# Performance work log

Measured on AMD Instinct MI355X. Metric: run time of the kernel, lower is better.

The kernel has to match this reference:

```python
import jax, jax.numpy as jnp
import numpy as np

T, B, D = 1024, 8, 1024
H, DH = 16, 64  # n_head, d_inner; H*DH == D
EPS = 1e-5


def setup_inputs() -> dict:
    key = jax.random.key(0)
    ks = jax.random.split(key, 8)
    q = jax.random.normal(ks[0], (T, B, D), dtype=jnp.float32)
    k = jax.random.normal(ks[1], (T, B, D), dtype=jnp.float32)
    v = jax.random.normal(ks[2], (T, B, D), dtype=jnp.float32)
    # causal mask: True where attention is disallowed (j > i)
    attn_mask = jnp.triu(jnp.ones((T, T), dtype=bool), k=1)
    Wq = jax.random.normal(ks[3], (D, H * DH), dtype=jnp.float32) * 0.02
    Wk = jax.random.normal(ks[4], (D, H * DH), dtype=jnp.float32) * 0.02
    Wv = jax.random.normal(ks[5], (D, H * DH), dtype=jnp.float32) * 0.02
    Wo = jax.random.normal(ks[6], (H * DH, D), dtype=jnp.float32) * 0.02
    gamma = jnp.ones((D,), dtype=jnp.float32)
    beta = jnp.zeros((D,), dtype=jnp.float32)
    return {"q": q, "k": k, "v": v, "attn_mask": attn_mask,
            "Wq": Wq, "Wk": Wk, "Wv": Wv, "Wo": Wo,
            "gamma": gamma, "beta": beta}


def _layer_norm(x, gamma, beta):
    mu = jnp.mean(x, axis=-1, keepdims=True)
    var = jnp.mean(jnp.square(x - mu), axis=-1, keepdims=True)
    return (x - mu) * jax.lax.rsqrt(var + EPS) * gamma + beta


def reference(q, k, v, attn_mask, Wq, Wk, Wv, Wo, gamma, beta):
    Tq, bsz, _ = q.shape
    Tk = k.shape[0]
    scale = 1.0 / (DH ** 0.5)
    # post-LN path (pre_lnorm=False): project raw inputs
    hq = (q @ Wq).reshape(Tq, bsz, H, DH)
    hk = (k @ Wk).reshape(Tk, bsz, H, DH)
    hv = (v @ Wv).reshape(Tk, bsz, H, DH)
    # explicit [Tq, Tk, B, H] score tensor, as in original
    score = jnp.einsum('ibhd,jbhd->ijbh', hq, hk) * scale
    score = jnp.where(attn_mask[:, :, None, None], -jnp.inf, score)
    prob = jax.nn.softmax(score, axis=1)  # softmax over key dim j
    vec = jnp.einsum('ijbh,jbhd->ibhd', prob, hv).reshape(Tq, bsz, H * DH)
    attn_out = vec @ Wo
    return _layer_norm(attn_out, gamma, beta)
```

## Files before the change

### kernel.cpp

```cpp
#include <hip/hip_runtime.h>
#include <hip/hip_bf16.h>


typedef __bf16 bf16x8 __attribute__((ext_vector_type(8)));
typedef float f32x4 __attribute__((ext_vector_type(4)));
typedef float f32x16 __attribute__((ext_vector_type(16)));
typedef unsigned short ushort8_t __attribute__((ext_vector_type(8)));

__device__ __forceinline__ unsigned short f2bf(float f) {
  unsigned int u = __builtin_bit_cast(unsigned int, f);
  u += 0x7FFFu + ((u >> 16) & 1u);
  return (unsigned short)(u >> 16);
}

__device__ __forceinline__ unsigned int cvt_pk_bf16(float lo, float hi) {
  unsigned int r;
  asm("v_cvt_pk_bf16_f32 %0, %1, %2" : "=v"(r) : "v"(lo), "v"(hi));
  return r;
}

__device__ __forceinline__ void gl2lds16(const unsigned short* g, unsigned short* l) {
  __builtin_amdgcn_global_load_lds(
      (const __attribute__((address_space(1))) void*)g,
      (__attribute__((address_space(3))) void*)l, 16, 0, 0);
}

template<int EPI>
__global__ __launch_bounds__(256)
void gemm_bf16(const unsigned short* __restrict__ A,
               const unsigned short* __restrict__ Bt,
               void* __restrict__ C)
{
  __shared__ __align__(16) unsigned short As[2][128 * 64];
  __shared__ __align__(16) unsigned short Bs[2][128 * 64];
  const int tid = threadIdx.x;
  const int lane = tid & 63, wid = tid >> 6;
  const int wr = wid >> 1, wc = wid & 1;
  const int l15 = lane & 15, l4 = lane >> 4;
  const int bm = blockIdx.x, bn = blockIdx.y;

  f32x4 acc[4][4];
#pragma unroll
  for (int m = 0; m < 4; ++m)
#pragma unroll
    for (int n = 0; n < 4; ++n)
      acc[m][n] = (f32x4){0.f, 0.f, 0.f, 0.f};

  const unsigned short* ga = A  + (size_t)bm * 128 * 1024 + (tid >> 3) * 1024 + (tid & 7) * 8;
  const unsigned short* gb = Bt + (size_t)bn * 128 * 1024 + (tid >> 3) * 1024 + (tid & 7) * 8;
  const int ldsoff = wid * 512;

#pragma unroll
  for (int i = 0; i < 4; ++i) {
    gl2lds16(ga + i * 32 * 1024, &As[0][ldsoff + i * 2048]);
    gl2lds16(gb + i * 32 * 1024, &Bs[0][ldsoff + i * 2048]);
  }

  int cur = 0;
  for (int kt = 0; kt < 1024; kt += 64) {
    __syncthreads();
    if (kt + 64 < 1024) {
#pragma unroll
      for (int i = 0; i < 4; ++i) {
        gl2lds16(ga + i * 32 * 1024 + kt + 64, &As[cur ^ 1][ldsoff + i * 2048]);
        gl2lds16(gb + i * 32 * 1024 + kt + 64, &Bs[cur ^ 1][ldsoff + i * 2048]);
      }
    }
#pragma unroll
    for (int kk = 0; kk < 2; ++kk) {
      bf16x8 af[4], bfr[4];
#pragma unroll
      for (int m = 0; m < 4; ++m)
        af[m] = *(const bf16x8*)(&As[cur][(wr * 64 + m * 16 + l15) * 64 + kk * 32 + l4 * 8]);
#pragma unroll
      for (int n = 0; n < 4; ++n)
        bfr[n] = *(const bf16x8*)(&Bs[cur][(wc * 64 + n * 16 + l15) * 64 + kk * 32 + l4 * 8]);
#pragma unroll
      for (int m = 0; m < 4; ++m)
#pragma unroll
        for (int n = 0; n < 4; ++n)
          acc[m][n] = __builtin_amdgcn_mfma_f32_16x16x32_bf16(af[m], bfr[n], acc[m][n], 0, 0, 0);
    }
    cur ^= 1;
  }

#pragma unroll
  for (int m = 0; m < 4; ++m)
#pragma unroll
    for (int n = 0; n < 4; ++n)
#pragma unroll
      for (int r = 0; r < 4; ++r) {
        int row = bm * 128 + wr * 64 + m * 16 + l4 * 4 + r;
        int col = bn * 128 + wc * 64 + n * 16 + l15;
        float v = acc[m][n][r];
        if constexpr (EPI == 2) {
          ((float*)C)[(size_t)row * 1024 + col] = v;
        } else {
          int t = row >> 3, b = row & 7;
          int h = col >> 6, dh = col & 63;
          size_t base = ((size_t)(b * 16 + h)) << 16;
          ((unsigned short*)C)[base + (size_t)dh * 1024 + t] = f2bf(v);
        }
      }
}

__global__ __launch_bounds__(256)
void gemm_qk(const unsigned short* __restrict__ Aq, const unsigned short* __restrict__ Ak,
             const unsigned short* __restrict__ Wq, const unsigned short* __restrict__ Wk,
             unsigned short* __restrict__ Cq, unsigned short* __restrict__ Ck)
{
  const int z = blockIdx.z;
  const unsigned short* A  = z ? Ak : Aq;
  const unsigned short* Bt = z ? Wk : Wq;
  unsigned short* C        = z ? Ck : Cq;
  __shared__ __align__(16) unsigned short As[128 * 64];
  __shared__ __align__(16) unsigned short Bs[128 * 64];
  const int tid = threadIdx.x;
  const int lane = tid & 63, wid = tid >> 6;
  const int wr = wid >> 1, wc = wid & 1;
  const int l15 = lane & 15, l4 = lane >> 4;
  const int bm = blockIdx.x, bn = blockIdx.y;

  f32x4 acc[4][4];
#pragma unroll
  for (int m = 0; m < 4; ++m)
#pragma unroll
    for (int n = 0; n < 4; ++n)
      acc[m][n] = (f32x4){0.f, 0.f, 0.f, 0.f};

  const unsigned short* ga = A  + (size_t)bm * 128 * 1024 + (tid >> 3) * 1024 + (tid & 7) * 8;
  const unsigned short* gb = Bt + (size_t)bn * 128 * 1024 + (tid >> 3) * 1024 + (tid & 7) * 8;
  unsigned short* la = As + wid * 512;
  unsigned short* lb = Bs + wid * 512;

  for (int kt = 0; kt < 1024; kt += 64) {
    if (kt) __syncthreads();
#pragma unroll
    for (int i = 0; i < 4; ++i) {
      gl2lds16(ga + i * 32 * 1024 + kt, la + i * 2048);
      gl2lds16(gb + i * 32 * 1024 + kt, lb + i * 2048);
    }
    __syncthreads();
#pragma unroll
    for (int kk = 0; kk < 2; ++kk) {
      bf16x8 af[4], bfr[4];
#pragma unroll
      for (int m = 0; m < 4; ++m)
        af[m] = *(const bf16x8*)(As + (wr * 64 + m * 16 + l15) * 64 + kk * 32 + l4 * 8);
#pragma unroll
      for (int n = 0; n < 4; ++n)
        bfr[n] = *(const bf16x8*)(Bs + (wc * 64 + n * 16 + l15) * 64 + kk * 32 + l4 * 8);
#pragma unroll
      for (int m = 0; m < 4; ++m)
#pragma unroll
        for (int n = 0; n < 4; ++n)
          acc[m][n] = __builtin_amdgcn_mfma_f32_16x16x32_bf16(af[m], bfr[n], acc[m][n], 0, 0, 0);
    }
  }

#pragma unroll
  for (int m = 0; m < 4; ++m)
#pragma unroll
    for (int n = 0; n < 4; ++n)
#pragma unroll
      for (int r = 0; r < 4; ++r) {
        int row = bm * 128 + wr * 64 + m * 16 + l4 * 4 + r;
        int col = bn * 128 + wc * 64 + n * 16 + l15;
        int t = row >> 3, b = row & 7;
        int h = col >> 6, dh = col & 63;
        size_t base = ((size_t)(b * 16 + h)) << 16;
        C[base + (size_t)t * 64 + dh] = f2bf(acc[m][n][r]);
      }
}

__global__ __launch_bounds__(256)
void conv_bf16(const float* __restrict__ in, unsigned short* __restrict__ out)
{
  size_t i = ((size_t)blockIdx.x * 256 + threadIdx.x) * 8;
  float4 a = *(const float4*)(in + i);
  float4 b = *(const float4*)(in + i + 4);
  ushort8_t o;
  o[0] = f2bf(a.x); o[1] = f2bf(a.y); o[2] = f2bf(a.z); o[3] = f2bf(a.w);
  o[4] = f2bf(b.x); o[5] = f2bf(b.y); o[6] = f2bf(b.z); o[7] = f2bf(b.w);
  *(ushort8_t*)(out + i) = o;
}

__global__ __launch_bounds__(256)
void conv2_bf16(const float* __restrict__ in0, const float* __restrict__ in1,
                unsigned short* __restrict__ out0, unsigned short* __restrict__ out1)
{
  const float* in = blockIdx.y ? in1 : in0;
  unsigned short* out = blockIdx.y ? out1 : out0;
  size_t i = ((size_t)blockIdx.x * 256 + threadIdx.x) * 8;
  float4 a = *(const float4*)(in + i);
  float4 b = *(const float4*)(in + i + 4);
  ushort8_t o;
  o[0] = f2bf(a.x); o[1] = f2bf(a.y); o[2] = f2bf(a.z); o[3] = f2bf(a.w);
  o[4] = f2bf(b.x); o[5] = f2bf(b.y); o[6] = f2bf(b.z); o[7] = f2bf(b.w);
  *(ushort8_t*)(out + i) = o;
}

__global__ __launch_bounds__(256)
void wconv4(const float* __restrict__ W0, const float* __restrict__ W1,
            const float* __restrict__ W2, const float* __restrict__ W3,
            unsigned short* __restrict__ T0, unsigned short* __restrict__ T1,
            unsigned short* __restrict__ T2, unsigned short* __restrict__ T3)
{
  const int y = blockIdx.y;
  const float* W = y == 0 ? W0 : y == 1 ? W1 : y == 2 ? W2 : W3;
  unsigned short* Wt = y == 0 ? T0 : y == 1 ? T1 : y == 2 ? T2 : T3;
  const float scale = (y == 0) ? 0.125f * 1.44269504088896f : 1.0f;
  int id = blockIdx.x * 256 + threadIdx.x;
  int n = id & 1023;
  int k0 = (id >> 10) << 3;
  ushort8_t o;
#pragma unroll
  for (int j = 0; j < 8; ++j)
    o[j] = f2bf(W[(size_t)(k0 + j) * 1024 + n] * scale);
  *(ushort8_t*)(Wt + (size_t)n * 1024 + k0) = o;
}

__global__ __launch_bounds__(256)
void flash_attn(const unsigned short* __restrict__ hq,
                const unsigned short* __restrict__ hk,
                const unsigned short* __restrict__ hvt,
                unsigned short* __restrict__ vec)
{
  __shared__ __align__(16) unsigned short Ks[2][64 * 64];
  __shared__ __align__(16) unsigned short Vs[2][64 * 64];
  const int tid = threadIdx.x;
  const int lane = tid & 63, wid = tid >> 6;
  const int l31 = lane & 31, h = lane >> 5;
  const int h8 = h * 8, h4 = h * 4;
  const int swz = l31 & 7;
  const int bid = blockIdx.x;
  const int xcd = bid & 7;
  const int i = bid >> 3;
  const int bh = (xcd << 4) | (i & 15);
  const int qb = 7 - (i >> 4);
  const int tau = qb * 4 + wid;
  const int b = bh >> 4, hh = bh & 15;
  const size_t base = (size_t)bh << 16;
  const int qrow = tau * 32 + l31;

  const int srow = wid * 8 + (lane >> 3);
  const int sc16 = (lane & 7) ^ (srow & 7);
  const unsigned short* gk = hk  + base + (size_t)srow * 64 + sc16 * 8;
  const unsigned short* gv = hvt + base + (size_t)srow * 1024 + sc16 * 8;
  const int ldst = wid * 512;

  bf16x8 qf[4];
#pragma unroll
  for (int ks = 0; ks < 4; ++ks)
    qf[ks] = *(const bf16x8*)(hq + base + (size_t)qrow * 64 + ks * 16 + h8);

  f32x16 of0, of1;
#pragma unroll
  for (int r = 0; r < 16; ++r) { of0[r] = 0.f; of1[r] = 0.f; }
  float mrun = -3.0e38f, lrun = 0.f;

  const int nblk = 2 * qb + 2;
  const int myend = (4 * qb + wid) >> 1;

  gl2lds16(gk,                 &Ks[0][ldst]);
  gl2lds16(gk + 32 * 64,       &Ks[0][2048 + ldst]);
  gl2lds16(gv,                 &Vs[0][ldst]);
  gl2lds16(gv + 32 * 1024,     &Vs[0][2048 + ldst]);

  int cur = 0;
  for (int kt = 0; kt < nblk; ++kt) {
    __syncthreads();
    if (kt + 1 < nblk) {
      const int kvb1 = (kt + 1) * 64;
      gl2lds16(gk + (size_t)kvb1 * 64,             &Ks[cur ^ 1][ldst]);
      gl2lds16(gk + (size_t)(kvb1 + 32) * 64,      &Ks[cur ^ 1][2048 + ldst]);
      gl2lds16(gv + kvb1,                          &Vs[cur ^ 1][ldst]);
      gl2lds16(gv + 32 * 1024 + kvb1,              &Vs[cur ^ 1][2048 + ldst]);
    }
    if (kt <= myend) {
      const int kvb = kt * 64;
      f32x16 sa, sb;
#pragma unroll
      for (int r = 0; r < 16; ++r) { sa[r] = 0.f; sb[r] = 0.f; }
      __builtin_amdgcn_s_setprio(1);
#pragma unroll
      for (int ks = 0; ks < 4; ++ks) {
        const int c = ((ks * 2 + h) ^ swz) << 3;
        bf16x8 kfa = *(const bf16x8*)(&Ks[cur][l31 * 64 + c]);
        bf16x8 kfb = *(const bf16x8*)(&Ks[cur][(32 + l31) * 64 + c]);
        sa = __builtin_amdgcn_mfma_f32_32x32x16_bf16(kfa, qf[ks], sa, 0, 0, 0);
        sb = __builtin_amdgcn_mfma_f32_32x32x16_bf16(kfb, qf[ks], sb, 0, 0, 0);
      }
      __builtin_amdgcn_s_setprio(0);
      if (kt == myend) {
#pragma unroll
        for (int r = 0; r < 16; ++r) {
          int kv = kvb + (r & 3) + 8 * (r >> 2) + h4;
          if (kv > qrow) sa[r] = -1.0e30f;
          if (kv + 32 > qrow) sb[r] = -1.0e30f;
        }
      }
      float mx[8];
#pragma unroll
      for (int g = 0; g < 4; ++g) {
        mx[g]     = fmaxf(fmaxf(sa[4 * g], sa[4 * g + 1]), fmaxf(sa[4 * g + 2], sa[4 * g + 3]));
        mx[4 + g] = fmaxf(fmaxf(sb[4 * g], sb[4 * g + 1]), fmaxf(sb[4 * g + 2], sb[4 * g + 3]));
      }
      mx[0] = fmaxf(mx[0], mx[1]); mx[2] = fmaxf(mx[2], mx[3]);
      mx[4] = fmaxf(mx[4], mx[5]); mx[6] = fmaxf(mx[6], mx[7]);
      float mloc = fmaxf(fmaxf(mx[0], mx[2]), fmaxf(mx[4], mx[6]));
      mloc = fmaxf(mloc, __shfl_xor(mloc, 32));
      if (!__all(mloc <= mrun + 8.0f)) {
        float mnew = fmaxf(mrun, mloc);
        float alpha = __builtin_amdgcn_exp2f(mrun - mnew);
        mrun = mnew;
        lrun *= alpha;
#pragma unroll
        for (int r = 0; r < 16; ++r) { of0[r] *= alpha; of1[r] *= alpha; }
      }
      bf16x8 pa[4];
      float lsum = 0.f;
#pragma unroll
      for (int s2 = 0; s2 < 4; ++s2) {
        float p0 = __builtin_amdgcn_exp2f(((s2 < 2) ? sa[8 * s2 + 0] : sb[8 * (s2 - 2) + 0]) - mrun);
        float p1 = __builtin_amdgcn_exp2f(((s2 < 2) ? sa[8 * s2 + 1] : sb[8 * (s2 - 2) + 1]) - mrun);
        float p2 = __builtin_amdgcn_exp2f(((s2 < 2) ? sa[8 * s2 + 2] : sb[8 * (s2 - 2) + 2]) - mrun);
        float p3 = __builtin_amdgcn_exp2f(((s2 < 2) ? sa[8 * s2 + 3] : sb[8 * (s2 - 2) + 3]) - mrun);
        float p4 = __builtin_amdgcn_exp2f(((s2 < 2) ? sa[8 * s2 + 4] : sb[8 * (s2 - 2) + 4]) - mrun);
        float p5 = __builtin_amdgcn_exp2f(((s2 < 2) ? sa[8 * s2 + 5] : sb[8 * (s2 - 2) + 5]) - mrun);
        float p6 = __builtin_amdgcn_exp2f(((s2 < 2) ? sa[8 * s2 + 6] : sb[8 * (s2 - 2) + 6]) - mrun);
        float p7 = __builtin_amdgcn_exp2f(((s2 < 2) ? sa[8 * s2 + 7] : sb[8 * (s2 - 2) + 7]) - mrun);
        lsum += (p0 + p1) + (p2 + p3) + ((p4 + p5) + (p6 + p7));
        uint4 w4 = make_uint4(cvt_pk_bf16(p0, p1), cvt_pk_bf16(p2, p3),
                              cvt_pk_bf16(p4, p5), cvt_pk_bf16(p6, p7));
        pa[s2] = __builtin_bit_cast(bf16x8, w4);
      }
      lsum += __shfl_xor(lsum, 32);
      lrun += lsum;
      __builtin_amdgcn_s_setprio(1);
#pragma unroll
      for (int s2 = 0; s2 < 4; ++s2) {
        const int c1 = (((2 * s2)     ^ swz) << 3) + h4;
        const int c2 = (((2 * s2 + 1) ^ swz) << 3) + h4;
        uint2 a1 = *(const uint2*)(&Vs[cur][l31 * 64 + c1]);
        uint2 a2 = *(const uint2*)(&Vs[cur][l31 * 64 + c2]);
        uint2 b1 = *(const uint2*)(&Vs[cur][(32 + l31) * 64 + c1]);
        uint2 b2 = *(const uint2*)(&Vs[cur][(32 + l31) * 64 + c2]);
        bf16x8 vf0 = __builtin_bit_cast(bf16x8, make_uint4(a1.x, a1.y, a2.x, a2.y));
        bf16x8 vf1 = __builtin_bit_cast(bf16x8, make_uint4(b1.x, b1.y, b2.x, b2.y));
        of0 = __builtin_amdgcn_mfma_f32_32x32x16_bf16(vf0, pa[s2], of0, 0, 0, 0);
        of1 = __builtin_amdgcn_mfma_f32_32x32x16_bf16(vf1, pa[s2], of1, 0, 0, 0);
      }
      __builtin_amdgcn_s_setprio(0);
    }
    cur ^= 1;
  }

  float rl = __builtin_amdgcn_rcpf(lrun);
  unsigned short* vout = vec + ((size_t)qrow * 8 + b) * 1024 + hh * 64;
#pragma unroll
  for (int g = 0; g < 4; ++g) {
    ushort4 o;
    o.x = f2bf(of0[g * 4 + 0] * rl); o.y = f2bf(of0[g * 4 + 1] * rl);
    o.z = f2bf(of0[g * 4 + 2] * rl); o.w = f2bf(of0[g * 4 + 3] * rl);
    *(ushort4*)(vout + 8 * g + h4) = o;
    o.x = f2bf(of1[g * 4 + 0] * rl); o.y = f2bf(of1[g * 4 + 1] * rl);
    o.z = f2bf(of1[g * 4 + 2] * rl); o.w = f2bf(of1[g * 4 + 3] * rl);
    *(ushort4*)(vout + 32 + 8 * g + h4) = o;
  }
}

__global__ __launch_bounds__(256)
void ln_inplace(float* __restrict__ x, const float* __restrict__ gamma,
                const float* __restrict__ beta)
{
  __shared__ float red[2][4];
  const int tid = threadIdx.x;
  const int lane = tid & 63, wid = tid >> 6;
  const size_t row = blockIdx.x;
  float4 v = *(const float4*)(x + row * 1024 + tid * 4);
  float s = v.x + v.y + v.z + v.w;
  float q = v.x * v.x + v.y * v.y + v.z * v.z + v.w * v.w;
#pragma unroll
  for (int m = 1; m <= 32; m <<= 1) {
    s += __shfl_xor(s, m);
    q += __shfl_xor(q, m);
  }
  if (lane == 0) { red[0][wid] = s; red[1][wid] = q; }
  __syncthreads();
  float ts = red[0][0] + red[0][1] + red[0][2] + red[0][3];
  float tq = red[1][0] + red[1][1] + red[1][2] + red[1][3];
  float mu = ts * (1.0f / 1024.0f);
  float var = tq * (1.0f / 1024.0f) - mu * mu;
  float rs = rsqrtf(var + 1e-5f);
  float4 g  = *(const float4*)(gamma + tid * 4);
  float4 bt = *(const float4*)(beta + tid * 4);
  v.x = (v.x - mu) * rs * g.x + bt.x;
  v.y = (v.y - mu) * rs * g.y + bt.y;
  v.z = (v.z - mu) * rs * g.z + bt.z;
  v.w = (v.w - mu) * rs * g.w + bt.w;
  *(float4*)(x + row * 1024 + tid * 4) = v;
}

extern "C" void kernel_launch(void* const* d_in, const int* in_sizes, int n_in,
                              void* d_out, int out_size, void* d_ws, size_t ws_size,
                              hipStream_t stream) {
  const float* q     = (const float*)d_in[0];
  const float* k     = (const float*)d_in[1];
  const float* v     = (const float*)d_in[2];
  const float* Wq    = (const float*)d_in[4];
  const float* Wk    = (const float*)d_in[5];
  const float* Wv    = (const float*)d_in[6];
  const float* Wo    = (const float*)d_in[7];
  const float* gamma = (const float*)d_in[8];
  const float* beta  = (const float*)d_in[9];

  unsigned short* ws = (unsigned short*)d_ws;
  const size_t MSZ = (size_t)8192 * 1024;
  unsigned short* hq   = ws;
  unsigned short* hk   = ws + MSZ;
  unsigned short* hvt  = ws + 2 * MSZ;
  unsigned short* tmp  = ws + 3 * MSZ;
  unsigned short* qb16 = ws + 4 * MSZ;
  unsigned short* WqT  = ws + 5 * MSZ;
  unsigned short* WkT  = WqT + 1048576;
  unsigned short* WvT  = WqT + 2097152;
  unsigned short* WoT  = WqT + 3145728;
  float* out = (float*)d_out;

  dim3 bb(256);
  dim3 gg(64, 8);
  wconv4<<<dim3(512, 4), bb, 0, stream>>>(Wq, Wk, Wv, Wo, WqT, WkT, WvT, WoT);

  conv_bf16<<<4096, bb, 0, stream>>>(v, tmp);
  gemm_bf16<1><<<gg, bb, 0, stream>>>(tmp, WvT, hvt);

  conv2_bf16<<<dim3(4096, 2), bb, 0, stream>>>(q, k, qb16, tmp);
  gemm_qk<<<dim3(64, 8, 2), bb, 0, stream>>>(qb16, tmp, WqT, WkT, hq, hk);

  flash_attn<<<1024, bb, 0, stream>>>(hq, hk, hvt, qb16);

  gemm_bf16<2><<<gg, bb, 0, stream>>>(qb16, WoT, out);
  ln_inplace<<<8192, bb, 0, stream>>>(out, gamma, beta);
}
```

Measured before the change: 210.6 us.

## Swizzle GEMM LDS layout and use 64-row tiles for V and output GEMMs

```diff
diff --git a/kernel.cpp b/kernel.cpp
--- a/kernel.cpp
+++ b/kernel.cpp
@@ -25,18 +25,22 @@
       (__attribute__((address_space(3))) void*)l, 16, 0, 0);
 }
 
-template<int EPI>
-__global__ __launch_bounds__(256)
-void gemm_bf16(const unsigned short* __restrict__ A,
-               const unsigned short* __restrict__ Bt,
-               void* __restrict__ C)
-{
-  __shared__ __align__(16) unsigned short As[2][128 * 64];
-  __shared__ __align__(16) unsigned short Bs[2][128 * 64];
+__global__ __launch_bounds__(256)
+void gemm_qk(const unsigned short* __restrict__ Aq, const unsigned short* __restrict__ Ak,
+             const unsigned short* __restrict__ Wq, const unsigned short* __restrict__ Wk,
+             unsigned short* __restrict__ Cq, unsigned short* __restrict__ Ck)
+{
+  const int z = blockIdx.z;
+  const unsigned short* A  = z ? Ak : Aq;
+  const unsigned short* Bt = z ? Wk : Wq;
+  unsigned short* C        = z ? Ck : Cq;
+  __shared__ __align__(16) unsigned short As[128 * 64];
+  __shared__ __align__(16) unsigned short Bs[128 * 64];
   const int tid = threadIdx.x;
   const int lane = tid & 63, wid = tid >> 6;
   const int wr = wid >> 1, wc = wid & 1;
   const int l15 = lane & 15, l4 = lane >> 4;
+  const int r7 = l15 & 7;
   const int bm = blockIdx.x, bn = blockIdx.y;
 
   f32x4 acc[4][4];
@@ -46,42 +50,36 @@
     for (int n = 0; n < 4; ++n)
       acc[m][n] = (f32x4){0.f, 0.f, 0.f, 0.f};
 
-  const unsigned short* ga = A  + (size_t)bm * 128 * 1024 + (tid >> 3) * 1024 + (tid & 7) * 8;
-  const unsigned short* gb = Bt + (size_t)bn * 128 * 1024 + (tid >> 3) * 1024 + (tid & 7) * 8;
-  const int ldsoff = wid * 512;
-
-#pragma unroll
-  for (int i = 0; i < 4; ++i) {
-    gl2lds16(ga + i * 32 * 1024, &As[0][ldsoff + i * 2048]);
-    gl2lds16(gb + i * 32 * 1024, &Bs[0][ldsoff + i * 2048]);
-  }
-
-  int cur = 0;
+  const int sc16 = (tid & 7) ^ ((tid >> 3) & 7);
+  const unsigned short* ga = A  + (size_t)bm * 128 * 1024 + (tid >> 3) * 1024 + sc16 * 8;
+  const unsigned short* gb = Bt + (size_t)bn * 128 * 1024 + (tid >> 3) * 1024 + sc16 * 8;
+  unsigned short* la = As + wid * 512;
+  unsigned short* lb = Bs + wid * 512;
+
   for (int kt = 0; kt < 1024; kt += 64) {
+    if (kt) __syncthreads();
+#pragma unroll
+    for (int i = 0; i < 4; ++i) {
+      gl2lds16(ga + i * 32 * 1024 + kt, la + i * 2048);
+      gl2lds16(gb + i * 32 * 1024 + kt, lb + i * 2048);
+    }
     __syncthreads();
-    if (kt + 64 < 1024) {
-#pragma unroll
-      for (int i = 0; i < 4; ++i) {
-        gl2lds16(ga + i * 32 * 1024 + kt + 64, &As[cur ^ 1][ldsoff + i * 2048]);
-        gl2lds16(gb + i * 32 * 1024 + kt + 64, &Bs[cur ^ 1][ldsoff + i * 2048]);
-      }
-    }
 #pragma unroll
     for (int kk = 0; kk < 2; ++kk) {
       bf16x8 af[4], bfr[4];
+      const int c = ((kk * 4 + l4) ^ r7) << 3;
 #pragma unroll
       for (int m = 0; m < 4; ++m)
-        af[m] = *(const bf16x8*)(&As[cur][(wr * 64 + m * 16 + l15) * 64 + kk * 32 + l4 * 8]);
+        af[m] = *(const bf16x8*)(As + (wr * 64 + m * 16 + l15) * 64 + c);
 #pragma unroll
       for (int n = 0; n < 4; ++n)
-        bfr[n] = *(const bf16x8*)(&Bs[cur][(wc * 64 + n * 16 + l15) * 64 + kk * 32 + l4 * 8]);
+        bfr[n] = *(const bf16x8*)(Bs + (wc * 64 + n * 16 + l15) * 64 + c);
 #pragma unroll
       for (int m = 0; m < 4; ++m)
 #pragma unroll
         for (int n = 0; n < 4; ++n)
           acc[m][n] = __builtin_amdgcn_mfma_f32_16x16x32_bf16(af[m], bfr[n], acc[m][n], 0, 0, 0);
     }
-    cur ^= 1;
   }
 
 #pragma unroll
@@ -91,6 +89,76 @@
 #pragma unroll
       for (int r = 0; r < 4; ++r) {
         int row = bm * 128 + wr * 64 + m * 16 + l4 * 4 + r;
+        int col = bn * 128 + wc * 64 + n * 16 + l15;
+        int t = row >> 3, b = row & 7;
+        int h = col >> 6, dh = col & 63;
+        size_t base = ((size_t)(b * 16 + h)) << 16;
+        C[base + (size_t)t * 64 + dh] = f2bf(acc[m][n][r]);
+      }
+}
+
+template<int EPI>
+__global__ __launch_bounds__(256)
+void gemm_small(const unsigned short* __restrict__ A,
+                const unsigned short* __restrict__ Bt,
+                void* __restrict__ C)
+{
+  __shared__ __align__(16) unsigned short As[64 * 64];
+  __shared__ __align__(16) unsigned short Bs[128 * 64];
+  const int tid = threadIdx.x;
+  const int lane = tid & 63, wid = tid >> 6;
+  const int wr = wid >> 1, wc = wid & 1;
+  const int l15 = lane & 15, l4 = lane >> 4;
+  const int r7 = l15 & 7;
+  const int bm = blockIdx.x, bn = blockIdx.y;
+
+  f32x4 acc[2][4];
+#pragma unroll
+  for (int m = 0; m < 2; ++m)
+#pragma unroll
+    for (int n = 0; n < 4; ++n)
+      acc[m][n] = (f32x4){0.f, 0.f, 0.f, 0.f};
+
+  const int sc16 = (tid & 7) ^ ((tid >> 3) & 7);
+  const unsigned short* ga = A  + (size_t)bm * 64 * 1024  + (tid >> 3) * 1024 + sc16 * 8;
+  const unsigned short* gb = Bt + (size_t)bn * 128 * 1024 + (tid >> 3) * 1024 + sc16 * 8;
+  unsigned short* la = As + wid * 512;
+  unsigned short* lb = Bs + wid * 512;
+
+  for (int kt = 0; kt < 1024; kt += 64) {
+    if (kt) __syncthreads();
+#pragma unroll
+    for (int i = 0; i < 2; ++i)
+      gl2lds16(ga + i * 32 * 1024 + kt, la + i * 2048);
+#pragma unroll
+    for (int i = 0; i < 4; ++i)
+      gl2lds16(gb + i * 32 * 1024 + kt, lb + i * 2048);
+    __syncthreads();
+#pragma unroll
+    for (int kk = 0; kk < 2; ++kk) {
+      const int c = ((kk * 4 + l4) ^ r7) << 3;
+      bf16x8 af[2], bfr[4];
+#pragma unroll
+      for (int m = 0; m < 2; ++m)
+        af[m] = *(const bf16x8*)(As + (wr * 32 + m * 16 + l15) * 64 + c);
+#pragma unroll
+      for (int n = 0; n < 4; ++n)
+        bfr[n] = *(const bf16x8*)(Bs + (wc * 64 + n * 16 + l15) * 64 + c);
+#pragma unroll
+      for (int m = 0; m < 2; ++m)
+#pragma unroll
+        for (int n = 0; n < 4; ++n)
+          acc[m][n] = __builtin_amdgcn_mfma_f32_16x16x32_bf16(af[m], bfr[n], acc[m][n], 0, 0, 0);
+    }
+  }
+
+#pragma unroll
+  for (int m = 0; m < 2; ++m)
+#pragma unroll
+    for (int n = 0; n < 4; ++n)
+#pragma unroll
+      for (int r = 0; r < 4; ++r) {
+        int row = bm * 64 + wr * 32 + m * 16 + l4 * 4 + r;
         int col = bn * 128 + wc * 64 + n * 16 + l15;
         float v = acc[m][n][r];
         if constexpr (EPI == 2) {
@@ -101,75 +169,6 @@
           size_t base = ((size_t)(b * 16 + h)) << 16;
           ((unsigned short*)C)[base + (size_t)dh * 1024 + t] = f2bf(v);
         }
-      }
-}
-
-__global__ __launch_bounds__(256)
-void gemm_qk(const unsigned short* __restrict__ Aq, const unsigned short* __restrict__ Ak,
-             const unsigned short* __restrict__ Wq, const unsigned short* __restrict__ Wk,
-             unsigned short* __restrict__ Cq, unsigned short* __restrict__ Ck)
-{
-  const int z = blockIdx.z;
-  const unsigned short* A  = z ? Ak : Aq;
-  const unsigned short* Bt = z ? Wk : Wq;
-  unsigned short* C        = z ? Ck : Cq;
-  __shared__ __align__(16) unsigned short As[128 * 64];
-  __shared__ __align__(16) unsigned short Bs[128 * 64];
-  const int tid = threadIdx.x;
-  const int lane = tid & 63, wid = tid >> 6;
-  const int wr = wid >> 1, wc = wid & 1;
-  const int l15 = lane & 15, l4 = lane >> 4;
-  const int bm = blockIdx.x, bn = blockIdx.y;
-
-  f32x4 acc[4][4];
-#pragma unroll
-  for (int m = 0; m < 4; ++m)
-#pragma unroll
-    for (int n = 0; n < 4; ++n)
-      acc[m][n] = (f32x4){0.f, 0.f, 0.f, 0.f};
-
-  const unsigned short* ga = A  + (size_t)bm * 128 * 1024 + (tid >> 3) * 1024 + (tid & 7) * 8;
-  const unsigned short* gb = Bt + (size_t)bn * 128 * 1024 + (tid >> 3) * 1024 + (tid & 7) * 8;
-  unsigned short* la = As + wid * 512;
-  unsigned short* lb = Bs + wid * 512;
-
-  for (int kt = 0; kt < 1024; kt += 64) {
-    if (kt) __syncthreads();
-#pragma unroll
-    for (int i = 0; i < 4; ++i) {
-      gl2lds16(ga + i * 32 * 1024 + kt, la + i * 2048);
-      gl2lds16(gb + i * 32 * 1024 + kt, lb + i * 2048);
-    }
-    __syncthreads();
-#pragma unroll
-    for (int kk = 0; kk < 2; ++kk) {
-      bf16x8 af[4], bfr[4];
-#pragma unroll
-      for (int m = 0; m < 4; ++m)
-        af[m] = *(const bf16x8*)(As + (wr * 64 + m * 16 + l15) * 64 + kk * 32 + l4 * 8);
-#pragma unroll
-      for (int n = 0; n < 4; ++n)
-        bfr[n] = *(const bf16x8*)(Bs + (wc * 64 + n * 16 + l15) * 64 + kk * 32 + l4 * 8);
-#pragma unroll
-      for (int m = 0; m < 4; ++m)
-#pragma unroll
-        for (int n = 0; n < 4; ++n)
-          acc[m][n] = __builtin_amdgcn_mfma_f32_16x16x32_bf16(af[m], bfr[n], acc[m][n], 0, 0, 0);
-    }
-  }
-
-#pragma unroll
-  for (int m = 0; m < 4; ++m)
-#pragma unroll
-    for (int n = 0; n < 4; ++n)
-#pragma unroll
-      for (int r = 0; r < 4; ++r) {
-        int row = bm * 128 + wr * 64 + m * 16 + l4 * 4 + r;
-        int col = bn * 128 + wc * 64 + n * 16 + l15;
-        int t = row >> 3, b = row & 7;
-        int h = col >> 6, dh = col & 63;
-        size_t base = ((size_t)(b * 16 + h)) << 16;
-        C[base + (size_t)t * 64 + dh] = f2bf(acc[m][n][r]);
       }
 }
 
@@ -262,20 +261,20 @@
   const int nblk = 2 * qb + 2;
   const int myend = (4 * qb + wid) >> 1;
 
-  gl2lds16(gk,                 &Ks[0][ldst]);
-  gl2lds16(gk + 32 * 64,       &Ks[0][2048 + ldst]);
-  gl2lds16(gv,                 &Vs[0][ldst]);
-  gl2lds16(gv + 32 * 1024,     &Vs[0][2048 + ldst]);
+  gl2lds16(gk,             &Ks[0][ldst]);
+  gl2lds16(gk + 32 * 64,   &Ks[0][2048 + ldst]);
+  gl2lds16(gv,             &Vs[0][ldst]);
+  gl2lds16(gv + 32 * 1024, &Vs[0][2048 + ldst]);
 
   int cur = 0;
   for (int kt = 0; kt < nblk; ++kt) {
     __syncthreads();
     if (kt + 1 < nblk) {
       const int kvb1 = (kt + 1) * 64;
-      gl2lds16(gk + (size_t)kvb1 * 64,             &Ks[cur ^ 1][ldst]);
-      gl2lds16(gk + (size_t)(kvb1 + 32) * 64,      &Ks[cur ^ 1][2048 + ldst]);
-      gl2lds16(gv + kvb1,                          &Vs[cur ^ 1][ldst]);
-      gl2lds16(gv + 32 * 1024 + kvb1,              &Vs[cur ^ 1][2048 + ldst]);
+      gl2lds16(gk + (size_t)kvb1 * 64,        &Ks[cur ^ 1][ldst]);
+      gl2lds16(gk + (size_t)(kvb1 + 32) * 64, &Ks[cur ^ 1][2048 + ldst]);
+      gl2lds16(gv + kvb1,                     &Vs[cur ^ 1][ldst]);
+      gl2lds16(gv + 32 * 1024 + kvb1,         &Vs[cur ^ 1][2048 + ldst]);
     }
     if (kt <= myend) {
       const int kvb = kt * 64;
@@ -429,17 +428,16 @@
   float* out = (float*)d_out;
 
   dim3 bb(256);
-  dim3 gg(64, 8);
   wconv4<<<dim3(512, 4), bb, 0, stream>>>(Wq, Wk, Wv, Wo, WqT, WkT, WvT, WoT);
 
   conv_bf16<<<4096, bb, 0, stream>>>(v, tmp);
-  gemm_bf16<1><<<gg, bb, 0, stream>>>(tmp, WvT, hvt);
+  gemm_small<1><<<dim3(128, 8), bb, 0, stream>>>(tmp, WvT, hvt);
 
   conv2_bf16<<<dim3(4096, 2), bb, 0, stream>>>(q, k, qb16, tmp);
   gemm_qk<<<dim3(64, 8, 2), bb, 0, stream>>>(qb16, tmp, WqT, WkT, hq, hk);
 
   flash_attn<<<1024, bb, 0, stream>>>(hq, hk, hvt, qb16);
 
-  gemm_bf16<2><<<gg, bb, 0, stream>>>(qb16, WoT, out);
+  gemm_small<2><<<dim3(128, 8), bb, 0, stream>>>(qb16, WoT, out);
   ln_inplace<<<8192, bb, 0, stream>>>(out, gamma, beta);
 }
```

Result: faster. 204.0 us (-3.2%).
